# Performance work log

Hardware: AMD Instinct MI355X
Metric: run time of the kernel (lower is better)

Reference implementation:

```python
import jax, jax.numpy as jnp
import numpy as np

B, S, HID = 2, 2048, 2048
NH, NKV, HD = 32, 8, 64
N_REP = NH // NKV
SCALING = HD ** -0.5
NEG_INF = -1e9


def rotate_half(x):
    x1, x2 = x[..., : x.shape[-1] // 2], x[..., x.shape[-1] // 2 :]
    return jnp.concatenate((-x2, x1), axis=-1)


def setup_inputs() -> dict:
    key = jax.random.key(0)
    ks = jax.random.split(key, 5)
    hidden_states = jax.random.normal(ks[0], (B, S, HID), dtype=jnp.float32)
    # real RoPE tables, theta=10000
    inv_freq = 1.0 / (10000.0 ** (jnp.arange(0, HD, 2, dtype=jnp.float32) / HD))
    freqs = jnp.arange(S, dtype=jnp.float32)[:, None] * inv_freq[None, :]  # [S, HD/2]
    emb = jnp.concatenate((freqs, freqs), axis=-1)  # [S, HD]
    cos = jnp.broadcast_to(jnp.cos(emb)[None], (B, S, HD))
    sin = jnp.broadcast_to(jnp.sin(emb)[None], (B, S, HD))
    # additive causal mask [B, 1, S, S]
    causal = jnp.tril(jnp.ones((S, S), dtype=bool))
    attention_mask = jnp.where(causal, 0.0, NEG_INF).astype(jnp.float32)
    attention_mask = jnp.broadcast_to(attention_mask[None, None], (B, 1, S, S))
    std = 0.02
    Wq = jax.random.normal(ks[1], (NH * HD, HID), dtype=jnp.float32) * std
    Wk = jax.random.normal(ks[2], (NKV * HD, HID), dtype=jnp.float32) * std
    Wv = jax.random.normal(ks[3], (NKV * HD, HID), dtype=jnp.float32) * std
    Wo = jax.random.normal(ks[4], (HID, NH * HD), dtype=jnp.float32) * std
    return {"hidden_states": hidden_states, "cos": cos, "sin": sin,
            "attention_mask": attention_mask, "Wq": Wq, "Wk": Wk, "Wv": Wv, "Wo": Wo}


def reference(hidden_states, cos, sin, attention_mask, Wq, Wk, Wv, Wo):
    b, s, _ = hidden_states.shape
    # projections (nn.Linear: y = x @ W.T), split heads -> [b, h, s, d]
    q = jnp.einsum("bsh,oh->bso", hidden_states, Wq).reshape(b, s, NH, HD).transpose(0, 2, 1, 3)
    k = jnp.einsum("bsh,oh->bso", hidden_states, Wk).reshape(b, s, NKV, HD).transpose(0, 2, 1, 3)
    v = jnp.einsum("bsh,oh->bso", hidden_states, Wv).reshape(b, s, NKV, HD).transpose(0, 2, 1, 3)
    # RoPE (cos/sin unsqueezed at dim 1)
    c, sn = cos[:, None], sin[:, None]
    q = q * c + rotate_half(q) * sn
    k = k * c + rotate_half(k) * sn
    # GQA repeat_kv
    k = jnp.repeat(k, N_REP, axis=1)
    v = jnp.repeat(v, N_REP, axis=1)
    # eager attention: QK^T -> +mask -> fp32 softmax -> V
    logits = jnp.einsum("bhqd,bhkd->bhqk", q, k) * SCALING + attention_mask
    attn_weights = jax.nn.softmax(logits.astype(jnp.float32), axis=-1).astype(q.dtype)
    attn_out = jnp.einsum("bhqk,bhkd->bhqd", attn_weights, v)
    attn_out = attn_out.transpose(0, 2, 1, 3).reshape(b, s, NH * HD)
    out = jnp.einsum("bso,ho->bsh", attn_out, Wo)
    return out, attn_weights
```

## Files before the change

### kernel.cpp

```cpp
#include <hip/hip_runtime.h>
#include <hip/hip_bf16.h>


typedef __bf16 bf16;
typedef bf16 bf16x8 __attribute__((ext_vector_type(8)));
typedef bf16 bf16x4 __attribute__((ext_vector_type(4)));
typedef float f32x4 __attribute__((ext_vector_type(4)));

#define B_   2
#define S_   2048
#define HID_ 2048
#define NH_  32
#define NKV_ 8
#define HD_  64
#define TOK_ (B_*S_)
#define QKVN 3072

__device__ __forceinline__ void gl_lds16(const bf16* g, bf16* l) {
  __builtin_amdgcn_global_load_lds(
      (const __attribute__((address_space(1))) unsigned int*)(g),
      (__attribute__((address_space(3))) unsigned int*)(l), 16, 0, 0);
}

__global__ __launch_bounds__(256) void cast_f32_bf16(const float* __restrict__ in,
                                                     bf16* __restrict__ out, int n4) {
  int i = blockIdx.x * 256 + threadIdx.x;
  if (i >= n4) return;
  f32x4 v = ((const f32x4*)in)[i];
  bf16x4 o;
  o[0] = (bf16)v[0]; o[1] = (bf16)v[1]; o[2] = (bf16)v[2]; o[3] = (bf16)v[3];
  ((bf16x4*)out)[i] = o;
}

__global__ __launch_bounds__(256) void cast_wqkv(const float* __restrict__ wq,
                                                 const float* __restrict__ wk,
                                                 const float* __restrict__ wv,
                                                 bf16* __restrict__ dst) {
  int i = blockIdx.x * 256 + threadIdx.x;
  const float* src; int off;
  if (i < 1048576)      { src = wq; off = i; }
  else if (i < 1310720) { src = wk; off = i - 1048576; }
  else                  { src = wv; off = i - 1310720; }
  f32x4 v = ((const f32x4*)src)[off];
  bf16x4 o;
  o[0] = (bf16)v[0]; o[1] = (bf16)v[1]; o[2] = (bf16)v[2]; o[3] = (bf16)v[3];
  ((bf16x4*)dst)[i] = o;
}

template<bool OUT_F32>
__global__ __launch_bounds__(256) void gemm_bt(const bf16* __restrict__ A,
                                               const bf16* __restrict__ Bm,
                                               void* __restrict__ Cout,
                                               int M, int N, int K) {
  __shared__ __align__(16) bf16 As[128 * 32];
  __shared__ __align__(16) bf16 Bs[128 * 32];
  const int tid  = threadIdx.x;
  const int wave = tid >> 6, lane = tid & 63;

  const int nwg = (int)(gridDim.x * gridDim.y);
  const int bid = (int)(blockIdx.y * gridDim.x + blockIdx.x);
  const int swz = (bid & 7) * (nwg >> 3) + (bid >> 3);
  const int bx = swz % (int)gridDim.x, by = swz / (int)gridDim.x;

  const int bm = by * 128, bn = bx * 128;
  const int wm = (wave >> 1) * 64, wn = (wave & 1) * 64;
  const int fr = lane & 15, fg = lane >> 4;

  const int r0   = wave * 32 + (lane >> 2);
  const int scol = (lane & 3) * 8;
  const bf16* ga0 = A  + (size_t)(bm + r0) * K + scol;
  const bf16* ga1 = ga0 + (size_t)16 * K;
  const bf16* gb0 = Bm + (size_t)(bn + r0) * K + scol;
  const bf16* gb1 = gb0 + (size_t)16 * K;
  bf16* lA0 = As + (wave * 32) * 32;
  bf16* lA1 = lA0 + 16 * 32;
  bf16* lB0 = Bs + (wave * 32) * 32;
  bf16* lB1 = lB0 + 16 * 32;

  f32x4 acc[4][4] = {};

  for (int k0 = 0; k0 < K; k0 += 32) {
    gl_lds16(ga0 + k0, lA0);
    gl_lds16(ga1 + k0, lA1);
    gl_lds16(gb0 + k0, lB0);
    gl_lds16(gb1 + k0, lB1);
    __syncthreads();
    bf16x8 af[4], bfv[4];
#pragma unroll
    for (int i = 0; i < 4; ++i) {
      af[i]  = *(const bf16x8*)&As[(wm + i * 16 + fr) * 32 + fg * 8];
      bfv[i] = *(const bf16x8*)&Bs[(wn + i * 16 + fr) * 32 + fg * 8];
    }
#pragma unroll
    for (int i = 0; i < 4; ++i)
#pragma unroll
      for (int j = 0; j < 4; ++j)
        acc[i][j] = __builtin_amdgcn_mfma_f32_16x16x32_bf16(af[i], bfv[j], acc[i][j], 0, 0, 0);
    __syncthreads();
  }

#pragma unroll
  for (int i = 0; i < 4; ++i)
#pragma unroll
    for (int j = 0; j < 4; ++j)
#pragma unroll
      for (int r = 0; r < 4; ++r) {
        int row = bm + wm + i * 16 + fg * 4 + r;
        int col = bn + wn + j * 16 + fr;
        float v = acc[i][j][r];
        if (OUT_F32) ((float*)Cout)[(size_t)row * N + col] = v;
        else         ((bf16*)Cout)[(size_t)row * N + col] = (bf16)v;
      }
}

__global__ __launch_bounds__(256) void rope_fused(bf16* __restrict__ qkv,
                                                  const float* __restrict__ cosp,
                                                  const float* __restrict__ sinp) {
  const int t = blockIdx.x;
  const int tid = threadIdx.x;
  const int d = tid & 31, g = tid >> 5;
  const float c = cosp[t * 64 + d];
  const float s = sinp[t * 64 + d];
  bf16* row = qkv + (size_t)t * QKVN;
#pragma unroll
  for (int i = 0; i < 4; ++i) {
    bf16* p = row + (g + i * 8) * 64 + d;
    float x1 = (float)p[0], x2 = (float)p[32];
    p[0]  = (bf16)(x1 * c - x2 * s);
    p[32] = (bf16)(x2 * c + x1 * s);
  }
  bf16* p = row + 2048 + g * 64 + d;
  float x1 = (float)p[0], x2 = (float)p[32];
  p[0]  = (bf16)(x1 * c - x2 * s);
  p[32] = (bf16)(x2 * c + x1 * s);
}

__global__ __launch_bounds__(256) void transpose_v(const bf16* __restrict__ v,
                                                   bf16* __restrict__ vT) {
  __shared__ __align__(16) bf16 t[64][72];
  const int bkv = blockIdx.y;
  const int b = bkv >> 3, kv = bkv & 7;
  const int s0 = blockIdx.x * 64;
  const int tid = threadIdx.x;
  const int r = tid >> 3, c = (tid & 7) * 8;
#pragma unroll
  for (int p = 0; p < 2; ++p) {
    int rr = r + p * 32;
    *(bf16x8*)&t[rr][c] = *(const bf16x8*)&v[(size_t)(b * S_ + s0 + rr) * QKVN + kv * 64 + c];
  }
  __syncthreads();
#pragma unroll
  for (int p = 0; p < 2; ++p) {
    int d = r + p * 32;
    bf16x8 o;
#pragma unroll
    for (int j = 0; j < 8; ++j) o[j] = t[c + j][d];
    *(bf16x8*)&vT[((size_t)bkv * 64 + d) * S_ + s0 + c] = o;
  }
}

__global__ __launch_bounds__(256, 4) void attn_kernel(const bf16* __restrict__ qkv,
                                                      const bf16* __restrict__ vT,
                                                      float* __restrict__ attnw,
                                                      bf16* __restrict__ attn_out)
{
  __shared__ __align__(16) bf16 Ks[64][72];
  __shared__ __align__(16) bf16 Vs[64][72];
  __shared__ __align__(16) bf16 Ps[4][16][72];

  const int tid  = threadIdx.x;
  const int wave = tid >> 6, lane = tid & 63;
  const int qt = blockIdx.x;
  const int bh = blockIdx.y;
  const int b = bh >> 5, h = bh & 31, kv = h >> 2;
  const int qLo = qt * 64;
  const int qHi = (31 - qt) * 64;
  const int NT  = 32 - qt;
  const int fr = lane & 15, fg = lane >> 4;
  const int rw = wave * 16;
  const int rt = rw + fg * 4;
  const int thr = rw + fr;

  bf16x8 aqL[2], aqH[2];
  {
    const bf16* qp = qkv + (size_t)(b * S_ + qLo + rw + fr) * QKVN + h * 64 + fg * 8;
    aqL[0] = *(const bf16x8*)qp;  aqL[1] = *(const bf16x8*)(qp + 32);
    qp = qkv + (size_t)(b * S_ + qHi + rw + fr) * QKVN + h * 64 + fg * 8;
    aqH[0] = *(const bf16x8*)qp;  aqH[1] = *(const bf16x8*)(qp + 32);
  }

  const int lr = tid >> 2;
  const int lc = (tid & 3) * 16;
  const bf16* kbase = qkv + (size_t)(b * S_) * QKVN + 2048 + kv * 64;
  const bf16* vbase = vT + (size_t)(b * NKV_ + kv) * 64 * S_;
  const bf16* kst = kbase + (size_t)lr * QKVN + lc;
  const bf16* vst = vbase + (size_t)lr * S_ + lc;

  float rsL = 0.f, rsH = 0.f;
  {
    bf16x8 kr0 = *(const bf16x8*)(kst);
    bf16x8 kr1 = *(const bf16x8*)(kst + 8);
    for (int jt = 0; jt < NT; ++jt) {
      __syncthreads();
      *(bf16x8*)&Ks[lr][lc]     = kr0;
      *(bf16x8*)&Ks[lr][lc + 8] = kr1;
      __syncthreads();
      if (jt + 1 < NT) {
        const bf16* p = kst + (size_t)(jt + 1) * 64 * QKVN;
        kr0 = *(const bf16x8*)(p);
        kr1 = *(const bf16x8*)(p + 8);
      }
      {
        f32x4 acc[4] = {};
#pragma unroll
        for (int nn = 0; nn < 4; ++nn) {
          bf16x8 bk0 = *(const bf16x8*)&Ks[nn*16 + fr][fg*8];
          bf16x8 bk1 = *(const bf16x8*)&Ks[nn*16 + fr][32 + fg*8];
          acc[nn] = __builtin_amdgcn_mfma_f32_16x16x32_bf16(bk0, aqH[0], acc[nn], 0, 0, 0);
          acc[nn] = __builtin_amdgcn_mfma_f32_16x16x32_bf16(bk1, aqH[1], acc[nn], 0, 0, 0);
        }
        if (jt < NT - 1) {
#pragma unroll
          for (int nn = 0; nn < 4; ++nn)
#pragma unroll
            for (int r = 0; r < 4; ++r) rsH += __expf(acc[nn][r] * 0.125f);
        } else {
#pragma unroll
          for (int nn = 0; nn < 4; ++nn)
#pragma unroll
            for (int r = 0; r < 4; ++r)
              if (nn * 16 + fg * 4 + r <= thr) rsH += __expf(acc[nn][r] * 0.125f);
        }
      }
      if (jt <= qt) {
        f32x4 acc[4] = {};
#pragma unroll
        for (int nn = 0; nn < 4; ++nn) {
          bf16x8 bk0 = *(const bf16x8*)&Ks[nn*16 + fr][fg*8];
          bf16x8 bk1 = *(const bf16x8*)&Ks[nn*16 + fr][32 + fg*8];
          acc[nn] = __builtin_amdgcn_mfma_f32_16x16x32_bf16(bk0, aqL[0], acc[nn], 0, 0, 0);
          acc[nn] = __builtin_amdgcn_mfma_f32_16x16x32_bf16(bk1, aqL[1], acc[nn], 0, 0, 0);
        }
        if (jt < qt) {
#pragma unroll
          for (int nn = 0; nn < 4; ++nn)
#pragma unroll
            for (int r = 0; r < 4; ++r) rsL += __expf(acc[nn][r] * 0.125f);
        } else {
#pragma unroll
          for (int nn = 0; nn < 4; ++nn)
#pragma unroll
            for (int r = 0; r < 4; ++r)
              if (nn * 16 + fg * 4 + r <= thr) rsL += __expf(acc[nn][r] * 0.125f);
        }
      }
    }
  }
  {
    float v = rsL;
    v += __shfl_xor(v, 16); v += __shfl_xor(v, 32);
    rsL = 1.0f / v;
    v = rsH;
    v += __shfl_xor(v, 16); v += __shfl_xor(v, 32);
    rsH = 1.0f / v;
  }

  {
    f32x4 z4 = {0.f, 0.f, 0.f, 0.f};
    const int zLo = (qt + 1) * 64;
    for (int rr = 0; rr < 16; ++rr) {
      size_t base = ((size_t)bh * S_ + qLo + rw + rr) * S_;
      for (int c = zLo + lane * 4; c < S_; c += 256)
        __builtin_nontemporal_store(z4, (f32x4*)&attnw[base + c]);
    }
    const int zHi = NT * 64;
    for (int rr = 0; rr < 16; ++rr) {
      size_t base = ((size_t)bh * S_ + qHi + rw + rr) * S_;
      for (int c = zHi + lane * 4; c < S_; c += 256)
        __builtin_nontemporal_store(z4, (f32x4*)&attnw[base + c]);
    }
  }

  f32x4 oL[4] = {}, oH[4] = {};
  {
    float* awpL = attnw + ((size_t)bh * S_ + qLo + rw + fr) * S_;
    float* awpH = attnw + ((size_t)bh * S_ + qHi + rw + fr) * S_;
    const int cb = fg * 4;
    bf16x8 kr0 = *(const bf16x8*)(kst);
    bf16x8 kr1 = *(const bf16x8*)(kst + 8);
    bf16x8 vr0 = *(const bf16x8*)(vst);
    bf16x8 vr1 = *(const bf16x8*)(vst + 8);
    for (int jt = 0; jt < NT; ++jt) {
      const int j0 = jt * 64;
      __syncthreads();
      *(bf16x8*)&Ks[lr][lc]     = kr0;
      *(bf16x8*)&Ks[lr][lc + 8] = kr1;
      *(bf16x8*)&Vs[lr][lc]     = vr0;
      *(bf16x8*)&Vs[lr][lc + 8] = vr1;
      __syncthreads();
      if (jt + 1 < NT) {
        const bf16* p = kst + (size_t)(jt + 1) * 64 * QKVN;
        kr0 = *(const bf16x8*)(p);
        kr1 = *(const bf16x8*)(p + 8);
        p = vst + (size_t)(jt + 1) * 64;
        vr0 = *(const bf16x8*)(p);
        vr1 = *(const bf16x8*)(p + 8);
      }
      {
        f32x4 acc[4] = {};
#pragma unroll
        for (int nn = 0; nn < 4; ++nn) {
          bf16x8 bk0 = *(const bf16x8*)&Ks[nn*16 + fr][fg*8];
          bf16x8 bk1 = *(const bf16x8*)&Ks[nn*16 + fr][32 + fg*8];
          acc[nn] = __builtin_amdgcn_mfma_f32_16x16x32_bf16(bk0, aqH[0], acc[nn], 0, 0, 0);
          acc[nn] = __builtin_amdgcn_mfma_f32_16x16x32_bf16(bk1, aqH[1], acc[nn], 0, 0, 0);
        }
        const bool diag = (jt == NT - 1);
#pragma unroll
        for (int nn = 0; nn < 4; ++nn) {
          f32x4 pv;
#pragma unroll
          for (int r = 0; r < 4; ++r) {
            float e = __expf(acc[nn][r] * 0.125f) * rsH;
            pv[r] = (diag && (nn * 16 + cb + r > thr)) ? 0.f : e;
            Ps[wave][fr][nn * 16 + cb + r] = (bf16)pv[r];
          }
          *(f32x4*)&awpH[j0 + nn * 16 + cb] = pv;
        }
        bf16x8 pa0 = *(const bf16x8*)&Ps[wave][fr][fg * 8];
        bf16x8 pa1 = *(const bf16x8*)&Ps[wave][fr][32 + fg * 8];
#pragma unroll
        for (int nn = 0; nn < 4; ++nn) {
          bf16x8 bv0 = *(const bf16x8*)&Vs[nn*16 + fr][fg*8];
          bf16x8 bv1 = *(const bf16x8*)&Vs[nn*16 + fr][32 + fg*8];
          oH[nn] = __builtin_amdgcn_mfma_f32_16x16x32_bf16(pa0, bv0, oH[nn], 0, 0, 0);
          oH[nn] = __builtin_amdgcn_mfma_f32_16x16x32_bf16(pa1, bv1, oH[nn], 0, 0, 0);
        }
      }
      if (jt <= qt) {
        f32x4 acc[4] = {};
#pragma unroll
        for (int nn = 0; nn < 4; ++nn) {
          bf16x8 bk0 = *(const bf16x8*)&Ks[nn*16 + fr][fg*8];
          bf16x8 bk1 = *(const bf16x8*)&Ks[nn*16 + fr][32 + fg*8];
          acc[nn] = __builtin_amdgcn_mfma_f32_16x16x32_bf16(bk0, aqL[0], acc[nn], 0, 0, 0);
          acc[nn] = __builtin_amdgcn_mfma_f32_16x16x32_bf16(bk1, aqL[1], acc[nn], 0, 0, 0);
        }
        const bool diag = (jt == qt);
#pragma unroll
        for (int nn = 0; nn < 4; ++nn) {
          f32x4 pv;
#pragma unroll
          for (int r = 0; r < 4; ++r) {
            float e = __expf(acc[nn][r] * 0.125f) * rsL;
            pv[r] = (diag && (nn * 16 + cb + r > thr)) ? 0.f : e;
            Ps[wave][fr][nn * 16 + cb + r] = (bf16)pv[r];
          }
          *(f32x4*)&awpL[j0 + nn * 16 + cb] = pv;
        }
        bf16x8 pa0 = *(const bf16x8*)&Ps[wave][fr][fg * 8];
        bf16x8 pa1 = *(const bf16x8*)&Ps[wave][fr][32 + fg * 8];
#pragma unroll
        for (int nn = 0; nn < 4; ++nn) {
          bf16x8 bv0 = *(const bf16x8*)&Vs[nn*16 + fr][fg*8];
          bf16x8 bv1 = *(const bf16x8*)&Vs[nn*16 + fr][32 + fg*8];
          oL[nn] = __builtin_amdgcn_mfma_f32_16x16x32_bf16(pa0, bv0, oL[nn], 0, 0, 0);
          oL[nn] = __builtin_amdgcn_mfma_f32_16x16x32_bf16(pa1, bv1, oL[nn], 0, 0, 0);
        }
      }
    }
  }

#pragma unroll
  for (int nn = 0; nn < 4; ++nn)
#pragma unroll
    for (int r = 0; r < 4; ++r) {
      int rowL = qLo + rt + r;
      int rowH = qHi + rt + r;
      attn_out[(size_t)(b * S_ + rowL) * (NH_*HD_) + h * 64 + nn * 16 + fr] = (bf16)oL[nn][r];
      attn_out[(size_t)(b * S_ + rowH) * (NH_*HD_) + h * 64 + nn * 16 + fr] = (bf16)oH[nn][r];
    }
}

extern "C" void kernel_launch(void* const* d_in, const int* in_sizes, int n_in,
                              void* d_out, int out_size, void* d_ws, size_t ws_size,
                              hipStream_t stream) {
  const float* hs   = (const float*)d_in[0];
  const float* cosp = (const float*)d_in[1];
  const float* sinp = (const float*)d_in[2];
  const float* Wq = (const float*)d_in[4];
  const float* Wk = (const float*)d_in[5];
  const float* Wv = (const float*)d_in[6];
  const float* Wo = (const float*)d_in[7];

  char* ws = (char*)d_ws;
  bf16* hs_b   = (bf16*)(ws);
  bf16* qkv_b  = (bf16*)(ws + (16u << 20));
  bf16* vT_b   = (bf16*)(ws + (40u << 20));
  bf16* ao_b   = (bf16*)(ws + (44u << 20));
  bf16* Wqkv_b = (bf16*)(ws + (60u << 20));
  bf16* Wo_b   = (bf16*)(ws + (72u << 20));

  float* outp  = (float*)d_out;
  float* attnw = outp + (size_t)TOK_ * HID_;

  cast_f32_bf16<<<(TOK_*HID_/4 + 255)/256, 256, 0, stream>>>(hs, hs_b, TOK_*HID_/4);
  cast_wqkv<<<(1572864 + 255)/256, 256, 0, stream>>>(Wq, Wk, Wv, Wqkv_b);
  cast_f32_bf16<<<(HID_*NH_*HD_/4 + 255)/256, 256, 0, stream>>>(Wo, Wo_b, HID_*NH_*HD_/4);

  gemm_bt<false><<<dim3(QKVN/128, TOK_/128), 256, 0, stream>>>(hs_b, Wqkv_b, qkv_b, TOK_, QKVN, HID_);

  rope_fused<<<TOK_, 256, 0, stream>>>(qkv_b, cosp, sinp);

  transpose_v<<<dim3(S_/64, B_*NKV_), 256, 0, stream>>>(qkv_b + 2560, vT_b);

  attn_kernel<<<dim3(S_/128, B_*NH_), 256, 0, stream>>>(qkv_b, vT_b, attnw, ao_b);

  gemm_bt<true><<<dim3(HID_/128, TOK_/128), 256, 0, stream>>>(ao_b, Wo_b, outp, TOK_, HID_, HID_);
}
```

Measured before the change: 446.0 us.

## Double-buffer K in row-sum pass, hoist zero-fill, vectorize P stores

The first attention pass, which only computes row sums, now keeps K in two shared-memory buffers. The next tile is written into the alternate buffer after compute, so only one barrier per iteration is needed instead of two. The zero-fill of the masked upper-triangle attention weights moves before the row-sum pass, so those stores can overlap with compute. Probability writes to shared memory are packed into 4-wide bf16 stores instead of scalar stores. The extra K buffer raises LDS use, which could reduce occupancy.

Result: faster. 433.3 us (-2.8%).

```diff
diff --git a/kernel.cpp b/kernel.cpp
--- a/kernel.cpp
+++ b/kernel.cpp
@@ -164,7 +164,7 @@
                                                       float* __restrict__ attnw,
                                                       bf16* __restrict__ attn_out)
 {
-  __shared__ __align__(16) bf16 Ks[64][72];
+  __shared__ __align__(16) bf16 Ks2[2][64][72];
   __shared__ __align__(16) bf16 Vs[64][72];
   __shared__ __align__(16) bf16 Ps[4][16][72];
 
@@ -196,15 +196,31 @@
   const bf16* kst = kbase + (size_t)lr * QKVN + lc;
   const bf16* vst = vbase + (size_t)lr * S_ + lc;
 
+  {
+    f32x4 z4 = {0.f, 0.f, 0.f, 0.f};
+    const int zLo = (qt + 1) * 64;
+    for (int rr = 0; rr < 16; ++rr) {
+      size_t base = ((size_t)bh * S_ + qLo + rw + rr) * S_;
+      for (int c = zLo + lane * 4; c < S_; c += 256)
+        __builtin_nontemporal_store(z4, (f32x4*)&attnw[base + c]);
+    }
+    const int zHi = NT * 64;
+    for (int rr = 0; rr < 16; ++rr) {
+      size_t base = ((size_t)bh * S_ + qHi + rw + rr) * S_;
+      for (int c = zHi + lane * 4; c < S_; c += 256)
+        __builtin_nontemporal_store(z4, (f32x4*)&attnw[base + c]);
+    }
+  }
+
   float rsL = 0.f, rsH = 0.f;
   {
     bf16x8 kr0 = *(const bf16x8*)(kst);
     bf16x8 kr1 = *(const bf16x8*)(kst + 8);
+    *(bf16x8*)&Ks2[0][lr][lc]     = kr0;
+    *(bf16x8*)&Ks2[0][lr][lc + 8] = kr1;
+    __syncthreads();
     for (int jt = 0; jt < NT; ++jt) {
-      __syncthreads();
-      *(bf16x8*)&Ks[lr][lc]     = kr0;
-      *(bf16x8*)&Ks[lr][lc + 8] = kr1;
-      __syncthreads();
+      const int cur = jt & 1;
       if (jt + 1 < NT) {
         const bf16* p = kst + (size_t)(jt + 1) * 64 * QKVN;
         kr0 = *(const bf16x8*)(p);
@@ -214,8 +230,8 @@
         f32x4 acc[4] = {};
 #pragma unroll
         for (int nn = 0; nn < 4; ++nn) {
-          bf16x8 bk0 = *(const bf16x8*)&Ks[nn*16 + fr][fg*8];
-          bf16x8 bk1 = *(const bf16x8*)&Ks[nn*16 + fr][32 + fg*8];
+          bf16x8 bk0 = *(const bf16x8*)&Ks2[cur][nn*16 + fr][fg*8];
+          bf16x8 bk1 = *(const bf16x8*)&Ks2[cur][nn*16 + fr][32 + fg*8];
           acc[nn] = __builtin_amdgcn_mfma_f32_16x16x32_bf16(bk0, aqH[0], acc[nn], 0, 0, 0);
           acc[nn] = __builtin_amdgcn_mfma_f32_16x16x32_bf16(bk1, aqH[1], acc[nn], 0, 0, 0);
         }
@@ -236,8 +252,8 @@
         f32x4 acc[4] = {};
 #pragma unroll
         for (int nn = 0; nn < 4; ++nn) {
-          bf16x8 bk0 = *(const bf16x8*)&Ks[nn*16 + fr][fg*8];
-          bf16x8 bk1 = *(const bf16x8*)&Ks[nn*16 + fr][32 + fg*8];
+          bf16x8 bk0 = *(const bf16x8*)&Ks2[cur][nn*16 + fr][fg*8];
+          bf16x8 bk1 = *(const bf16x8*)&Ks2[cur][nn*16 + fr][32 + fg*8];
           acc[nn] = __builtin_amdgcn_mfma_f32_16x16x32_bf16(bk0, aqL[0], acc[nn], 0, 0, 0);
           acc[nn] = __builtin_amdgcn_mfma_f32_16x16x32_bf16(bk1, aqL[1], acc[nn], 0, 0, 0);
         }
@@ -253,6 +269,11 @@
             for (int r = 0; r < 4; ++r)
               if (nn * 16 + fg * 4 + r <= thr) rsL += __expf(acc[nn][r] * 0.125f);
         }
+      }
+      if (jt + 1 < NT) {
+        *(bf16x8*)&Ks2[cur ^ 1][lr][lc]     = kr0;
+        *(bf16x8*)&Ks2[cur ^ 1][lr][lc + 8] = kr1;
+        __syncthreads();
       }
     }
   }
@@ -263,22 +284,6 @@
     v = rsH;
     v += __shfl_xor(v, 16); v += __shfl_xor(v, 32);
     rsH = 1.0f / v;
-  }
-
-  {
-    f32x4 z4 = {0.f, 0.f, 0.f, 0.f};
-    const int zLo = (qt + 1) * 64;
-    for (int rr = 0; rr < 16; ++rr) {
-      size_t base = ((size_t)bh * S_ + qLo + rw + rr) * S_;
-      for (int c = zLo + lane * 4; c < S_; c += 256)
-        __builtin_nontemporal_store(z4, (f32x4*)&attnw[base + c]);
-    }
-    const int zHi = NT * 64;
-    for (int rr = 0; rr < 16; ++rr) {
-      size_t base = ((size_t)bh * S_ + qHi + rw + rr) * S_;
-      for (int c = zHi + lane * 4; c < S_; c += 256)
-        __builtin_nontemporal_store(z4, (f32x4*)&attnw[base + c]);
-    }
   }
 
   f32x4 oL[4] = {}, oH[4] = {};
@@ -293,8 +298,8 @@
     for (int jt = 0; jt < NT; ++jt) {
       const int j0 = jt * 64;
       __syncthreads();
-      *(bf16x8*)&Ks[lr][lc]     = kr0;
-      *(bf16x8*)&Ks[lr][lc + 8] = kr1;
+      *(bf16x8*)&Ks2[0][lr][lc]     = kr0;
+      *(bf16x8*)&Ks2[0][lr][lc + 8] = kr1;
       *(bf16x8*)&Vs[lr][lc]     = vr0;
       *(bf16x8*)&Vs[lr][lc + 8] = vr1;
       __syncthreads();
@@ -310,8 +315,8 @@
         f32x4 acc[4] = {};
 #pragma unroll
         for (int nn = 0; nn < 4; ++nn) {
-          bf16x8 bk0 = *(const bf16x8*)&Ks[nn*16 + fr][fg*8];
-          bf16x8 bk1 = *(const bf16x8*)&Ks[nn*16 + fr][32 + fg*8];
+          bf16x8 bk0 = *(const bf16x8*)&Ks2[0][nn*16 + fr][fg*8];
+          bf16x8 bk1 = *(const bf16x8*)&Ks2[0][nn*16 + fr][32 + fg*8];
           acc[nn] = __builtin_amdgcn_mfma_f32_16x16x32_bf16(bk0, aqH[0], acc[nn], 0, 0, 0);
           acc[nn] = __builtin_amdgcn_mfma_f32_16x16x32_bf16(bk1, aqH[1], acc[nn], 0, 0, 0);
         }
@@ -319,13 +324,15 @@
 #pragma unroll
         for (int nn = 0; nn < 4; ++nn) {
           f32x4 pv;
+          bf16x4 pb;
 #pragma unroll
           for (int r = 0; r < 4; ++r) {
             float e = __expf(acc[nn][r] * 0.125f) * rsH;
             pv[r] = (diag && (nn * 16 + cb + r > thr)) ? 0.f : e;
-            Ps[wave][fr][nn * 16 + cb + r] = (bf16)pv[r];
+            pb[r] = (bf16)pv[r];
           }
           *(f32x4*)&awpH[j0 + nn * 16 + cb] = pv;
+          *(bf16x4*)&Ps[wave][fr][nn * 16 + cb] = pb;
         }
         bf16x8 pa0 = *(const bf16x8*)&Ps[wave][fr][fg * 8];
         bf16x8 pa1 = *(const bf16x8*)&Ps[wave][fr][32 + fg * 8];
@@ -341,8 +348,8 @@
         f32x4 acc[4] = {};
 #pragma unroll
         for (int nn = 0; nn < 4; ++nn) {
-          bf16x8 bk0 = *(const bf16x8*)&Ks[nn*16 + fr][fg*8];
-          bf16x8 bk1 = *(const bf16x8*)&Ks[nn*16 + fr][32 + fg*8];
+          bf16x8 bk0 = *(const bf16x8*)&Ks2[0][nn*16 + fr][fg*8];
+          bf16x8 bk1 = *(const bf16x8*)&Ks2[0][nn*16 + fr][32 + fg*8];
           acc[nn] = __builtin_amdgcn_mfma_f32_16x16x32_bf16(bk0, aqL[0], acc[nn], 0, 0, 0);
           acc[nn] = __builtin_amdgcn_mfma_f32_16x16x32_bf16(bk1, aqL[1], acc[nn], 0, 0, 0);
         }
@@ -350,13 +357,15 @@
 #pragma unroll
         for (int nn = 0; nn < 4; ++nn) {
           f32x4 pv;
+          bf16x4 pb;
 #pragma unroll
           for (int r = 0; r < 4; ++r) {
             float e = __expf(acc[nn][r] * 0.125f) * rsL;
             pv[r] = (diag && (nn * 16 + cb + r > thr)) ? 0.f : e;
-            Ps[wave][fr][nn * 16 + cb + r] = (bf16)pv[r];
+            pb[r] = (bf16)pv[r];
           }
           *(f32x4*)&awpL[j0 + nn * 16 + cb] = pv;
+          *(bf16x4*)&Ps[wave][fr][nn * 16 + cb] = pb;
         }
         bf16x8 pa0 = *(const bf16x8*)&Ps[wave][fr][fg * 8];
         bf16x8 pa1 = *(const bf16x8*)&Ps[wave][fr][32 + fg * 8];
```
